# Kernel optimization log

Hardware: AMD Instinct MI355X
Metric: run time of the kernel (lower is better)

Reference implementation:

```python
import jax, jax.numpy as jnp
import numpy as np

BLOCK = 16
FP4_LEVELS = jnp.array([0.0, 0.5, 1.0, 1.5, 2.0, 3.0, 4.0, 6.0], dtype=jnp.float32)
FP4_MIDS = jnp.array([0.25, 0.75, 1.25, 1.75, 2.5, 3.5, 5.0], dtype=jnp.float32)
E4M3_MAX = 448.0
FP4_MAX = 6.0


def _fp4_round(v):
    # round-to-nearest onto signed E2M1 grid {0,.5,1,1.5,2,3,4,6}
    a = jnp.minimum(jnp.abs(v), FP4_MAX)
    idx = jnp.searchsorted(FP4_MIDS, a, side='right')
    return jnp.sign(v) * FP4_LEVELS[idx]


def _encode_scale(block_amax, global_amax):
    # two-level NVFP4 scaling: block scale stored as FP8 E4M3 relative to global scale
    g_scale = global_amax / (E4M3_MAX * FP4_MAX)
    s = block_amax / FP4_MAX
    s_q = jnp.clip(s / g_scale, 0.0, E4M3_MAX).astype(jnp.float8_e4m3fn).astype(jnp.float32) * g_scale
    return s_q


def nvfp4_qdq_1d(x, block=BLOCK):
    # blockwise fake-quant along the last dim (activations)
    sh = x.shape
    xb = x.reshape(sh[:-1] + (sh[-1] // block, block))
    g_amax = jnp.max(jnp.abs(x))
    b_amax = jnp.max(jnp.abs(xb), axis=-1, keepdims=True)
    s = _encode_scale(b_amax, g_amax)
    s_safe = jnp.where(s > 0, s, 1.0)
    dq = _fp4_round(xb / s_safe) * s
    return dq.reshape(sh)


def nvfp4_qdq_2d(w, block=BLOCK):
    # (16,16) 2D block fake-quant for the weight [out, in]
    O, I = w.shape
    wb = w.reshape(O // block, block, I // block, block)
    g_amax = jnp.max(jnp.abs(w))
    b_amax = jnp.max(jnp.abs(wb), axis=(1, 3), keepdims=True)
    s = _encode_scale(b_amax, g_amax)
    s_safe = jnp.where(s > 0, s, 1.0)
    dq = _fp4_round(wb / s_safe) * s
    return dq.reshape(O, I)


def setup_inputs() -> dict:
    key = jax.random.key(0)
    kx, kw = jax.random.split(key)
    B, S, D_IN, D_OUT = 4, 2048, 4096, 4096
    x = jax.random.normal(kx, (B, S, D_IN), dtype=jnp.float32)
    weight = jax.random.normal(kw, (D_OUT, D_IN), dtype=jnp.float32) * 0.02
    bias = jnp.zeros((D_OUT,), dtype=jnp.float32)
    return {"x": x, "weight": weight, "bias": bias}


def reference(x, weight, bias):
    x_hat = nvfp4_qdq_1d(x)
    x_ste = x + jax.lax.stop_gradient(x_hat - x)
    w_hat = nvfp4_qdq_2d(weight)
    w_ste = weight + jax.lax.stop_gradient(w_hat - weight)
    y = jnp.einsum('bsi,oi->bso', x_ste, w_ste)
    return y + bias
```

## Files before the change

### kernel.cpp

```cpp
#include <hip/hip_runtime.h>

typedef unsigned short u16;
typedef unsigned int u32;
typedef __bf16 bf16x8 __attribute__((ext_vector_type(8)));
typedef float f32x4 __attribute__((ext_vector_type(4)));


__device__ __forceinline__ float e4m3_rne(float r) {
  if (r < 0.015625f) {
    return rintf(r * 512.0f) * (1.0f / 512.0f);
  }
  u32 u = __float_as_uint(r);
  u32 lsb = (u >> 20) & 1u;
  u += 0x7FFFFu + lsb;
  u &= 0xFFF00000u;
  return __uint_as_float(u);
}

__device__ __forceinline__ float fp4_level(float a, const float* t) {
  return a < t[3] ? (a < t[1] ? (a < t[0] ? 0.0f : 0.5f)
                              : (a < t[2] ? 1.0f : 1.5f))
                  : (a < t[5] ? (a < t[4] ? 2.0f : 3.0f)
                              : (a < t[6] ? 4.0f : 6.0f));
}

__device__ __forceinline__ void gload_lds16(const u16* g, void* l) {
  __builtin_amdgcn_global_load_lds(
      (const __attribute__((address_space(1))) void*)g,
      (__attribute__((address_space(3))) void*)l, 16, 0, 0);
}


__global__ void __launch_bounds__(256) amax_part_kernel(const float4* __restrict__ p,
                                                        int n4, float* __restrict__ part) {
  float m = 0.0f;
  int stride = gridDim.x * 256;
  for (int i = blockIdx.x * 256 + threadIdx.x; i < n4; i += stride) {
    float4 v = p[i];
    m = fmaxf(m, fmaxf(fmaxf(fabsf(v.x), fabsf(v.y)), fmaxf(fabsf(v.z), fabsf(v.w))));
  }
#pragma unroll
  for (int o = 32; o > 0; o >>= 1) m = fmaxf(m, __shfl_xor(m, o));
  __shared__ float red[4];
  int wid = threadIdx.x >> 6, lane = threadIdx.x & 63;
  if (lane == 0) red[wid] = m;
  __syncthreads();
  if (threadIdx.x == 0)
    part[blockIdx.x] = fmaxf(fmaxf(red[0], red[1]), fmaxf(red[2], red[3]));
}

__global__ void __launch_bounds__(256) finalize_kernel(const float* __restrict__ px,
                                                       const float* __restrict__ pw,
                                                       float* __restrict__ scal,
                                                       int nx, int nw) {
  int tid = threadIdx.x;
  float mx = 0.0f, mw = 0.0f;
  for (int i = tid; i < nx; i += 256) mx = fmaxf(mx, px[i]);
  for (int i = tid; i < nw; i += 256) mw = fmaxf(mw, pw[i]);
#pragma unroll
  for (int o = 32; o > 0; o >>= 1) {
    mx = fmaxf(mx, __shfl_xor(mx, o));
    mw = fmaxf(mw, __shfl_xor(mw, o));
  }
  __shared__ float rx[4], rw[4];
  int wid = tid >> 6, lane = tid & 63;
  if (lane == 0) { rx[wid] = mx; rw[wid] = mw; }
  __syncthreads();
  if (tid == 0) {
    scal[0] = fmaxf(fmaxf(rx[0], rx[1]), fmaxf(rx[2], rx[3]));
    scal[1] = fmaxf(fmaxf(rw[0], rw[1]), fmaxf(rw[2], rw[3]));
  }
}


__global__ void __launch_bounds__(256) quant_x_kernel(const float* __restrict__ x,
                                                      const float* __restrict__ scal,
                                                      u16* __restrict__ q, int nblk) {
  int b = blockIdx.x * 256 + threadIdx.x;
  if (b >= nblk) return;
  const float4* px = (const float4*)(x + (size_t)b * 16);
  float4 v[4];
  v[0] = px[0]; v[1] = px[1]; v[2] = px[2]; v[3] = px[3];
  float am = 0.0f;
  const float* vf = (const float*)v;
#pragma unroll
  for (int i = 0; i < 16; ++i) am = fmaxf(am, fabsf(vf[i]));

  float g = scal[0] / 2688.0f;
  float ratio = fminf(fmaxf((am / 6.0f) / g, 0.0f), 448.0f);
  float sq = e4m3_rne(ratio);
  float s = sq * g;
  float ss = s > 0.0f ? s : 1.0f;
  float t[7] = {0.25f * ss, 0.75f * ss, 1.25f * ss, 1.75f * ss,
                2.5f * ss, 3.5f * ss, 5.0f * ss};

  union { u16 h[16]; uint4 v4[2]; } ou;
#pragma unroll
  for (int i = 0; i < 16; ++i) {
    float qv = copysignf(fp4_level(fabsf(vf[i]), t) * sq, vf[i]);
    ou.h[i] = (u16)(__float_as_uint(qv) >> 16);
  }
  uint4* qd = (uint4*)(q + (size_t)b * 16);
  qd[0] = ou.v4[0];
  qd[1] = ou.v4[1];
}


__global__ void __launch_bounds__(256) quant_w_kernel(const float* __restrict__ w,
                                                      const float* __restrict__ scal,
                                                      u16* __restrict__ q, int ntc, int K) {
  int wav = blockIdx.x * 4 + (threadIdx.x >> 6);
  int lane = threadIdx.x & 63;
  int tr = wav / ntc, tc = wav % ntc;
  int r = lane >> 2, c = (lane & 3) * 4;
  size_t off = (size_t)(tr * 16 + r) * K + tc * 16 + c;
  float4 v = *(const float4*)(w + off);
  float am = fmaxf(fmaxf(fabsf(v.x), fabsf(v.y)), fmaxf(fabsf(v.z), fabsf(v.w)));
#pragma unroll
  for (int o = 32; o > 0; o >>= 1) am = fmaxf(am, __shfl_xor(am, o));

  float g = scal[1] / 2688.0f;
  float ratio = fminf(fmaxf((am / 6.0f) / g, 0.0f), 448.0f);
  float sq = e4m3_rne(ratio);
  float s = sq * g;
  float ss = s > 0.0f ? s : 1.0f;
  float t[7] = {0.25f * ss, 0.75f * ss, 1.25f * ss, 1.75f * ss,
                2.5f * ss, 3.5f * ss, 5.0f * ss};

  float vf[4] = {v.x, v.y, v.z, v.w};
  union { u16 h[4]; uint2 v2; } ou;
#pragma unroll
  for (int i = 0; i < 4; ++i) {
    float qv = copysignf(fp4_level(fabsf(vf[i]), t) * sq, vf[i]);
    ou.h[i] = (u16)(__float_as_uint(qv) >> 16);
  }
  *(uint2*)(q + off) = ou.v2;
}


#define BM 256
#define BN 256
#define BK 64

__global__ void __launch_bounds__(512, 2) gemm_kernel(const u16* __restrict__ A,
                                                      const u16* __restrict__ B,
                                                      const float* __restrict__ bias,
                                                      const float* __restrict__ scal,
                                                      float* __restrict__ out,
                                                      int M, int N, int K) {
  extern __shared__ char lds[];
  const int tid = threadIdx.x;
  const int wid = tid >> 6, lane = tid & 63;
  const int fr = lane & 15, fc = lane >> 4;
  const int wm = wid >> 2, wn = wid & 3;
  const int sw = (fr & 7) << 4;

  int nwg = gridDim.x, bid = blockIdx.x;
  int q8 = nwg >> 3, r8 = nwg & 7;
  int xcd = bid & 7, loc = bid >> 3;
  int wg = (xcd < r8 ? xcd * (q8 + 1) : r8 * (q8 + 1) + (xcd - r8) * q8) + loc;
  int ntn = N / BN;
  int tm = wg / ntn, tn = wg % ntn;
  int brow = tm * BM, bcol = tn * BN;

  const int srow = tid >> 3;
  const int scol = ((((tid & 7) << 4) ^ ((srow & 7) << 4)) >> 1);
  const u16* gA = A + (size_t)(brow + srow) * K + scol;
  const u16* gB = B + (size_t)(bcol + srow) * K + scol;
  const size_t K64 = (size_t)K * 64;
  const int ldsOff = wid << 10;

#define STAGE_A(bufbase, ktoff) do {                                         \
    _Pragma("unroll") for (int s_ = 0; s_ < 4; ++s_)                         \
      gload_lds16(gA + (size_t)s_ * K64 + (ktoff), (bufbase) + s_ * 8192 + ldsOff); \
  } while (0)
#define STAGE_B(bufbase, ktoff) do {                                         \
    _Pragma("unroll") for (int s_ = 0; s_ < 4; ++s_)                         \
      gload_lds16(gB + (size_t)s_ * K64 + (ktoff), (bufbase) + s_ * 8192 + ldsOff); \
  } while (0)

#define LOAD_A(dst, qm)                                                      \
  _Pragma("unroll") for (int j_ = 0; j_ < 4; ++j_)                           \
  _Pragma("unroll") for (int k_ = 0; k_ < 2; ++k_)                           \
    dst[j_][k_] = *(const bf16x8*)(abuf + ((wm * 128 + (qm) * 64 + j_ * 16 + fr) * 128 \
                                           + (((fc << 4) + (k_ << 6)) ^ sw)));
#define LOAD_B(dst, qn)                                                      \
  _Pragma("unroll") for (int j_ = 0; j_ < 2; ++j_)                           \
  _Pragma("unroll") for (int k_ = 0; k_ < 2; ++k_)                           \
    dst[j_][k_] = *(const bf16x8*)(bbuf + ((wn * 64 + (qn) * 32 + j_ * 16 + fr) * 128 \
                                           + (((fc << 4) + (k_ << 6)) ^ sw)));

#define MMA(qm, qn, af, bf)                                                  \
  _Pragma("unroll") for (int j_ = 0; j_ < 4; ++j_)                           \
  _Pragma("unroll") for (int n_ = 0; n_ < 2; ++n_)                           \
  _Pragma("unroll") for (int k_ = 0; k_ < 2; ++k_)                           \
    acc[(qm) * 4 + j_][(qn) * 2 + n_] = __builtin_amdgcn_mfma_f32_16x16x32_bf16( \
        af[j_][k_], bf[n_][k_], acc[(qm) * 4 + j_][(qn) * 2 + n_], 0, 0, 0);

#define PHASE_MID()                                          \
  __builtin_amdgcn_s_barrier();                              \
  asm volatile("s_waitcnt lgkmcnt(0)" ::: "memory");         \
  __builtin_amdgcn_sched_barrier(0);                         \
  __builtin_amdgcn_s_setprio(1);
#define PHASE_END()                                          \
  __builtin_amdgcn_s_setprio(0);                             \
  __builtin_amdgcn_s_barrier();

  f32x4 acc[8][4];
  f32x4 zero = {0.0f, 0.0f, 0.0f, 0.0f};
#pragma unroll
  for (int m = 0; m < 8; ++m)
#pragma unroll
    for (int n = 0; n < 4; ++n) acc[m][n] = zero;

  const int NT = K / BK;

  STAGE_A(lds, 0);
  STAGE_B(lds + 32768, 0);
  asm volatile("s_waitcnt vmcnt(0)" ::: "memory");
  __builtin_amdgcn_s_barrier();

  bf16x8 a[4][2], b0[2][2], b1[2][2];
  int cur = 0;
  for (int t = 0; t < NT; ++t) {
    const char* abuf = lds + cur * 65536;
    const char* bbuf = abuf + 32768;
    char* sbuf = lds + (cur ^ 1) * 65536;
    const bool pf = (t + 1 < NT);
    const int ktn = (t + 1) * BK;

    LOAD_A(a, 0);
    LOAD_B(b0, 0);
    if (pf) STAGE_A(sbuf, ktn);
    PHASE_MID();
    MMA(0, 0, a, b0);
    PHASE_END();

    LOAD_B(b1, 1);
    if (pf) STAGE_B(sbuf + 32768, ktn);
    PHASE_MID();
    MMA(0, 1, a, b1);
    PHASE_END();

    LOAD_A(a, 1);
    PHASE_MID();
    MMA(1, 1, a, b1);
    PHASE_END();

    __builtin_amdgcn_s_setprio(1);
    MMA(1, 0, a, b0);
    __builtin_amdgcn_s_setprio(0);
    asm volatile("s_waitcnt vmcnt(0)" ::: "memory");
    __builtin_amdgcn_s_barrier();
    cur ^= 1;
  }

  float gs = (scal[0] / 2688.0f) * (scal[1] / 2688.0f);
#pragma unroll
  for (int n = 0; n < 4; ++n) {
    int col = bcol + wn * 64 + n * 16 + fr;
    float bv = bias[col];
#pragma unroll
    for (int m = 0; m < 8; ++m) {
      int row0 = brow + wm * 128 + m * 16 + (fc << 2);
      f32x4 v = acc[m][n];
#pragma unroll
      for (int j = 0; j < 4; ++j)
        out[(size_t)(row0 + j) * N + col] = v[j] * gs + bv;
    }
  }
}


extern "C" void kernel_launch(void* const* d_in, const int* in_sizes, int n_in,
                              void* d_out, int out_size, void* d_ws, size_t ws_size,
                              hipStream_t stream) {
  const float* x = (const float*)d_in[0];
  const float* w = (const float*)d_in[1];
  const float* bias = (const float*)d_in[2];
  float* out = (float*)d_out;

  const int DOUT = in_sizes[2];
  const int K = in_sizes[1] / DOUT;
  const int M = in_sizes[0] / K;
  const int N = DOUT;

  float* scal = (float*)d_ws;
  float* px = (float*)((char*)d_ws + 256);
  float* pw = px + 1024;
  u16* qw = (u16*)((char*)d_ws + 8192);
  u16* qx = (u16*)((char*)d_ws + 8192 + (size_t)N * K * 2);

  amax_part_kernel<<<1024, 256, 0, stream>>>((const float4*)x, (M * K) / 4, px);
  amax_part_kernel<<<512, 256, 0, stream>>>((const float4*)w, (N * K) / 4, pw);
  finalize_kernel<<<1, 256, 0, stream>>>(px, pw, scal, 1024, 512);

  int nblk = (M * K) / 16;
  quant_x_kernel<<<(nblk + 255) / 256, 256, 0, stream>>>(x, scal, qx, nblk);

  int ntiles = (N / 16) * (K / 16);
  quant_w_kernel<<<ntiles / 4, 256, 0, stream>>>(w, scal, qw, K / 16, K);

  gemm_kernel<<<(M / BM) * (N / BN), 512, 131072, stream>>>(qx, qw, bias, scal, out,
                                                            M, N, K);
}
```

Before: 348.6 us.

## Replace direct global-to-LDS loads with register-staged prefetch in GEMM mainloop

Drops the global_load_lds direct-to-LDS staging in the bf16 MFMA GEMM. Tiles are now loaded into registers (uint4), then written to the swizzled LDS buffer in the third phase, and the final loop iteration is peeled. The end-of-iteration vmcnt wait and barrier are removed, and B fragments are reloaded before the last MMA so the register budget stays manageable. The aim is to hide global latency behind MFMA work without a full vmcnt stall per tile, at the cost of extra VGPRs and LDS write instructions.

New measurement: 458.0 us. 1.31x slower.

```diff
diff --git a/kernel.cpp b/kernel.cpp
--- a/kernel.cpp
+++ b/kernel.cpp
@@ -22,12 +22,6 @@
                               : (a < t[2] ? 1.0f : 1.5f))
                   : (a < t[5] ? (a < t[4] ? 2.0f : 3.0f)
                               : (a < t[6] ? 4.0f : 6.0f));
-}
-
-__device__ __forceinline__ void gload_lds16(const u16* g, void* l) {
-  __builtin_amdgcn_global_load_lds(
-      (const __attribute__((address_space(1))) void*)g,
-      (__attribute__((address_space(3))) void*)l, 16, 0, 0);
 }
 
 
@@ -164,19 +158,25 @@
   int brow = tm * BM, bcol = tn * BN;
 
   const int srow = tid >> 3;
-  const int scol = ((((tid & 7) << 4) ^ ((srow & 7) << 4)) >> 1);
-  const u16* gA = A + (size_t)(brow + srow) * K + scol;
-  const u16* gB = B + (size_t)(bcol + srow) * K + scol;
+  const u16* gA = A + (size_t)(brow + srow) * K + (tid & 7) * 8;
+  const u16* gB = B + (size_t)(bcol + srow) * K + (tid & 7) * 8;
   const size_t K64 = (size_t)K * 64;
-  const int ldsOff = wid << 10;
-
-#define STAGE_A(bufbase, ktoff) do {                                         \
-    _Pragma("unroll") for (int s_ = 0; s_ < 4; ++s_)                         \
-      gload_lds16(gA + (size_t)s_ * K64 + (ktoff), (bufbase) + s_ * 8192 + ldsOff); \
+  const int wOff = srow * 128 + (((tid & 7) << 4) ^ ((srow & 7) << 4));
+
+  uint4 ra[4], rb[4];
+#define GLOAD_A(kt) do {                                                     \
+    _Pragma("unroll") for (int c_ = 0; c_ < 4; ++c_)                         \
+      ra[c_] = *(const uint4*)(gA + (size_t)c_ * K64 + (kt));                \
   } while (0)
-#define STAGE_B(bufbase, ktoff) do {                                         \
-    _Pragma("unroll") for (int s_ = 0; s_ < 4; ++s_)                         \
-      gload_lds16(gB + (size_t)s_ * K64 + (ktoff), (bufbase) + s_ * 8192 + ldsOff); \
+#define GLOAD_B(kt) do {                                                     \
+    _Pragma("unroll") for (int c_ = 0; c_ < 4; ++c_)                         \
+      rb[c_] = *(const uint4*)(gB + (size_t)c_ * K64 + (kt));                \
+  } while (0)
+#define SWRITE(bufbase) do {                                                 \
+    _Pragma("unroll") for (int c_ = 0; c_ < 4; ++c_)                         \
+      *(uint4*)((bufbase) + c_ * 8192 + wOff) = ra[c_];                      \
+    _Pragma("unroll") for (int c_ = 0; c_ < 4; ++c_)                         \
+      *(uint4*)((bufbase) + 32768 + c_ * 8192 + wOff) = rb[c_];              \
   } while (0)
 
 #define LOAD_A(dst, qm)                                                      \
@@ -204,7 +204,8 @@
   __builtin_amdgcn_s_setprio(1);
 #define PHASE_END()                                          \
   __builtin_amdgcn_s_setprio(0);                             \
-  __builtin_amdgcn_s_barrier();
+  __builtin_amdgcn_s_barrier();                              \
+  __builtin_amdgcn_sched_barrier(0);
 
   f32x4 acc[8][4];
   f32x4 zero = {0.0f, 0.0f, 0.0f, 0.0f};
@@ -215,44 +216,69 @@
 
   const int NT = K / BK;
 
-  STAGE_A(lds, 0);
-  STAGE_B(lds + 32768, 0);
-  asm volatile("s_waitcnt vmcnt(0)" ::: "memory");
-  __builtin_amdgcn_s_barrier();
+  GLOAD_A(0);
+  GLOAD_B(0);
+  SWRITE(lds);
+  __syncthreads();
 
   bf16x8 a[4][2], b0[2][2], b1[2][2];
   int cur = 0;
-  for (int t = 0; t < NT; ++t) {
+  for (int t = 0; t < NT - 1; ++t) {
     const char* abuf = lds + cur * 65536;
     const char* bbuf = abuf + 32768;
     char* sbuf = lds + (cur ^ 1) * 65536;
-    const bool pf = (t + 1 < NT);
     const int ktn = (t + 1) * BK;
 
     LOAD_A(a, 0);
     LOAD_B(b0, 0);
-    if (pf) STAGE_A(sbuf, ktn);
+    GLOAD_A(ktn);
     PHASE_MID();
     MMA(0, 0, a, b0);
     PHASE_END();
 
     LOAD_B(b1, 1);
-    if (pf) STAGE_B(sbuf + 32768, ktn);
+    GLOAD_B(ktn);
     PHASE_MID();
     MMA(0, 1, a, b1);
     PHASE_END();
 
     LOAD_A(a, 1);
+    SWRITE(sbuf);
     PHASE_MID();
     MMA(1, 1, a, b1);
     PHASE_END();
 
+    LOAD_B(b0, 0);
+    asm volatile("s_waitcnt lgkmcnt(0)" ::: "memory");
+    __builtin_amdgcn_sched_barrier(0);
     __builtin_amdgcn_s_setprio(1);
     MMA(1, 0, a, b0);
     __builtin_amdgcn_s_setprio(0);
-    asm volatile("s_waitcnt vmcnt(0)" ::: "memory");
-    __builtin_amdgcn_s_barrier();
     cur ^= 1;
+  }
+
+  {
+    const char* abuf = lds + cur * 65536;
+    const char* bbuf = abuf + 32768;
+    LOAD_A(a, 0);
+    LOAD_B(b0, 0);
+    PHASE_MID();
+    MMA(0, 0, a, b0);
+    PHASE_END();
+    LOAD_B(b1, 1);
+    PHASE_MID();
+    MMA(0, 1, a, b1);
+    PHASE_END();
+    LOAD_A(a, 1);
+    PHASE_MID();
+    MMA(1, 1, a, b1);
+    PHASE_END();
+    LOAD_B(b0, 0);
+    asm volatile("s_waitcnt lgkmcnt(0)" ::: "memory");
+    __builtin_amdgcn_sched_barrier(0);
+    __builtin_amdgcn_s_setprio(1);
+    MMA(1, 0, a, b0);
+    __builtin_amdgcn_s_setprio(0);
   }
 
   float gs = (scal[0] / 2688.0f) * (scal[1] / 2688.0f);
```

## Stage global-to-LDS loads in finer chunks two tiles ahead with partial vmcnt waits

Applied to the files above, without the earlier changes.

Splits the A and B global-to-LDS staging into per-chunk loads. Part of the next-next tile's data is issued into the buffer currently being consumed, once its rows are no longer needed. Waits become partial vmcnt waits instead of full drains, and LDS reads use inline ds_read_b128 with immediate offsets to cut address arithmetic. B staging also gets a new row layout matching the per-wave quadrant reads. This deepens the prefetch to hide global latency, at the cost of delicate correctness reasoning around buffer reuse and wait counts.

After: 335.2 us. 1.04x faster.

```diff
diff --git a/kernel.cpp b/kernel.cpp
--- a/kernel.cpp
+++ b/kernel.cpp
@@ -166,29 +166,45 @@
   const int srow = tid >> 3;
   const int scol = ((((tid & 7) << 4) ^ ((srow & 7) << 4)) >> 1);
   const u16* gA = A + (size_t)(brow + srow) * K + scol;
-  const u16* gB = B + (size_t)(bcol + srow) * K + scol;
-  const size_t K64 = (size_t)K * 64;
-  const int ldsOff = wid << 10;
-
-#define STAGE_A(bufbase, ktoff) do {                                         \
-    _Pragma("unroll") for (int s_ = 0; s_ < 4; ++s_)                         \
-      gload_lds16(gA + (size_t)s_ * K64 + (ktoff), (bufbase) + s_ * 8192 + ldsOff); \
-  } while (0)
-#define STAGE_B(bufbase, ktoff) do {                                         \
-    _Pragma("unroll") for (int s_ = 0; s_ < 4; ++s_)                         \
-      gload_lds16(gB + (size_t)s_ * K64 + (ktoff), (bufbase) + s_ * 8192 + ldsOff); \
-  } while (0)
-
-#define LOAD_A(dst, qm)                                                      \
-  _Pragma("unroll") for (int j_ = 0; j_ < 4; ++j_)                           \
-  _Pragma("unroll") for (int k_ = 0; k_ < 2; ++k_)                           \
-    dst[j_][k_] = *(const bf16x8*)(abuf + ((wm * 128 + (qm) * 64 + j_ * 16 + fr) * 128 \
-                                           + (((fc << 4) + (k_ << 6)) ^ sw)));
-#define LOAD_B(dst, qn)                                                      \
-  _Pragma("unroll") for (int j_ = 0; j_ < 2; ++j_)                           \
-  _Pragma("unroll") for (int k_ = 0; k_ < 2; ++k_)                           \
-    dst[j_][k_] = *(const bf16x8*)(bbuf + ((wn * 64 + (qn) * 32 + j_ * 16 + fr) * 128 \
-                                           + (((fc << 4) + (k_ << 6)) ^ sw)));
+  const int rowB0 = (srow & 31) + (srow >> 5) * 128;
+  const u16* gB = B + (size_t)(bcol + rowB0) * K + scol;
+  const size_t K64r = (size_t)K * 64;
+  const size_t K32r = (size_t)K * 32;
+  const int ldsAoff = wid << 10;
+  const int ldsBoff = ((wid & 3) << 10) + ((wid >> 2) << 14);
+
+#define STAGE_A1(buf, kt, c) \
+  gload_lds16(gA + (size_t)(c) * K64r + (kt), (buf) + (c) * 8192 + ldsAoff)
+#define STAGE_B1(buf, kt, c) \
+  gload_lds16(gB + (size_t)(c) * K32r + (kt), (buf) + 32768 + (c) * 4096 + ldsBoff)
+
+  const u32 ldsbase = (u32)(uintptr_t)(__attribute__((address_space(3))) char*)lds;
+  const u32 cb0 = (u32)((fc << 4) ^ sw);
+  const u32 cb1 = cb0 ^ 64u;
+  const u32 aB0 = ldsbase + (u32)((wm * 128 + fr) * 128) + cb0;
+  const u32 aB1 = ldsbase + (u32)((wm * 128 + fr) * 128) + cb1;
+  const u32 bB0 = ldsbase + 32768u + (u32)((wn * 64 + fr) * 128) + cb0;
+  const u32 bB1 = ldsbase + 32768u + (u32)((wn * 64 + fr) * 128) + cb1;
+
+#define DSR(dst, ad, off) \
+  asm volatile("ds_read_b128 %0, %1 offset:" off : "=v"(dst) : "v"(ad))
+
+#define LOAD_A0() do { \
+  DSR(a[0][0], aC0, "0");    DSR(a[0][1], aC1, "0");    \
+  DSR(a[1][0], aC0, "2048"); DSR(a[1][1], aC1, "2048"); \
+  DSR(a[2][0], aC0, "4096"); DSR(a[2][1], aC1, "4096"); \
+  DSR(a[3][0], aC0, "6144"); DSR(a[3][1], aC1, "6144"); } while (0)
+#define LOAD_A1() do { \
+  DSR(a[0][0], aC0, "8192");  DSR(a[0][1], aC1, "8192");  \
+  DSR(a[1][0], aC0, "10240"); DSR(a[1][1], aC1, "10240"); \
+  DSR(a[2][0], aC0, "12288"); DSR(a[2][1], aC1, "12288"); \
+  DSR(a[3][0], aC0, "14336"); DSR(a[3][1], aC1, "14336"); } while (0)
+#define LOAD_B0() do { \
+  DSR(b0[0][0], bC0, "0");    DSR(b0[0][1], bC1, "0");    \
+  DSR(b0[1][0], bC0, "2048"); DSR(b0[1][1], bC1, "2048"); } while (0)
+#define LOAD_B1() do { \
+  DSR(b1[0][0], bC0, "4096"); DSR(b1[0][1], bC1, "4096"); \
+  DSR(b1[1][0], bC0, "6144"); DSR(b1[1][1], bC1, "6144"); } while (0)
 
 #define MMA(qm, qn, af, bf)                                                  \
   _Pragma("unroll") for (int j_ = 0; j_ < 4; ++j_)                           \
@@ -204,7 +220,8 @@
   __builtin_amdgcn_s_setprio(1);
 #define PHASE_END()                                          \
   __builtin_amdgcn_s_setprio(0);                             \
-  __builtin_amdgcn_s_barrier();
+  __builtin_amdgcn_s_barrier();                              \
+  __builtin_amdgcn_sched_barrier(0);
 
   f32x4 acc[8][4];
   f32x4 zero = {0.0f, 0.0f, 0.0f, 0.0f};
@@ -215,43 +232,54 @@
 
   const int NT = K / BK;
 
-  STAGE_A(lds, 0);
-  STAGE_B(lds + 32768, 0);
-  asm volatile("s_waitcnt vmcnt(0)" ::: "memory");
+  STAGE_A1(lds, 0, 0); STAGE_A1(lds, 0, 1); STAGE_A1(lds, 0, 2); STAGE_A1(lds, 0, 3);
+  STAGE_B1(lds, 0, 0); STAGE_B1(lds, 0, 1); STAGE_B1(lds, 0, 2); STAGE_B1(lds, 0, 3);
+  STAGE_A1(lds + 65536, BK, 0); STAGE_A1(lds + 65536, BK, 2);
+  STAGE_B1(lds + 65536, BK, 1); STAGE_B1(lds + 65536, BK, 3);
+  asm volatile("s_waitcnt vmcnt(4)" ::: "memory");
   __builtin_amdgcn_s_barrier();
 
   bf16x8 a[4][2], b0[2][2], b1[2][2];
   int cur = 0;
   for (int t = 0; t < NT; ++t) {
-    const char* abuf = lds + cur * 65536;
-    const char* bbuf = abuf + 32768;
-    char* sbuf = lds + (cur ^ 1) * 65536;
-    const bool pf = (t + 1 < NT);
-    const int ktn = (t + 1) * BK;
-
-    LOAD_A(a, 0);
-    LOAD_B(b0, 0);
-    if (pf) STAGE_A(sbuf, ktn);
+    const u32 bo = (u32)(cur << 16);
+    const u32 aC0 = aB0 + bo, aC1 = aB1 + bo;
+    const u32 bC0 = bB0 + bo, bC1 = bB1 + bo;
+    char* bq = lds + (cur ^ 1) * 65536;
+    char* bp = lds + cur * 65536;
+    const int kt1 = (t + 1) * BK, kt2 = (t + 2) * BK;
+    const int st1 = (t + 1 < NT), st2 = (t + 2 < NT);
+
+    LOAD_A0();
+    LOAD_B0();
+    if (st1) { STAGE_A1(bq, kt1, 1); STAGE_A1(bq, kt1, 3); }
     PHASE_MID();
     MMA(0, 0, a, b0);
     PHASE_END();
 
-    LOAD_B(b1, 1);
-    if (pf) STAGE_B(sbuf + 32768, ktn);
+    LOAD_B1();
+    if (st1) { STAGE_B1(bq, kt1, 0); STAGE_B1(bq, kt1, 2); }
     PHASE_MID();
     MMA(0, 1, a, b1);
-    PHASE_END();
-
-    LOAD_A(a, 1);
+    __builtin_amdgcn_s_setprio(0);
+    asm volatile("s_waitcnt vmcnt(4)" ::: "memory");
+    __builtin_amdgcn_s_barrier();
+    __builtin_amdgcn_sched_barrier(0);
+
+    LOAD_A1();
+    if (st2) { STAGE_A1(bp, kt2, 0); STAGE_A1(bp, kt2, 2); }
     PHASE_MID();
     MMA(1, 1, a, b1);
     PHASE_END();
 
+    if (st2) { STAGE_B1(bp, kt2, 1); STAGE_B1(bp, kt2, 3); }
     __builtin_amdgcn_s_setprio(1);
     MMA(1, 0, a, b0);
     __builtin_amdgcn_s_setprio(0);
-    asm volatile("s_waitcnt vmcnt(0)" ::: "memory");
+    if (st2) asm volatile("s_waitcnt vmcnt(4)" ::: "memory");
+    else     asm volatile("s_waitcnt vmcnt(0)" ::: "memory");
     __builtin_amdgcn_s_barrier();
+    __builtin_amdgcn_sched_barrier(0);
     cur ^= 1;
   }
 
```

## Restructure GEMM mainloop into 4-stage BK=32 pipeline with register double-buffering

Applied to the files above, without the earlier changes.

Halves the K tile to 32 and uses four LDS stages, prefetching two tiles ahead with partial vmcnt waits instead of draining all loads every iteration. LDS reads for the next tile are issued with inline ds_read_b128 into a second register set, between the two MMA halves, so fragment loads overlap with MFMA work. It also switches to a new swizzled LDS layout with two rows per 128-byte line. The aim is to remove per-iteration barrier stalls and global-load latency exposure, at the cost of more register pressure and more barriers per unit of K.

After: 359.4 us. 3.1% more time.

```diff
diff --git a/kernel.cpp b/kernel.cpp
--- a/kernel.cpp
+++ b/kernel.cpp
@@ -140,7 +140,7 @@
 
 #define BM 256
 #define BN 256
-#define BK 64
+#define BK 32
 
 __global__ void __launch_bounds__(512, 2) gemm_kernel(const u16* __restrict__ A,
                                                       const u16* __restrict__ B,
@@ -153,7 +153,6 @@
   const int wid = tid >> 6, lane = tid & 63;
   const int fr = lane & 15, fc = lane >> 4;
   const int wm = wid >> 2, wn = wid & 3;
-  const int sw = (fr & 7) << 4;
 
   int nwg = gridDim.x, bid = blockIdx.x;
   int q8 = nwg >> 3, r8 = nwg & 7;
@@ -163,48 +162,72 @@
   int tm = wg / ntn, tn = wg % ntn;
   int brow = tm * BM, bcol = tn * BN;
 
-  const int srow = tid >> 3;
-  const int scol = ((((tid & 7) << 4) ^ ((srow & 7) << 4)) >> 1);
-  const u16* gA = A + (size_t)(brow + srow) * K + scol;
-  const u16* gB = B + (size_t)(bcol + srow) * K + scol;
-  const size_t K64 = (size_t)K * 64;
-  const int ldsOff = wid << 10;
-
-#define STAGE_A(bufbase, ktoff) do {                                         \
-    _Pragma("unroll") for (int s_ = 0; s_ < 4; ++s_)                         \
-      gload_lds16(gA + (size_t)s_ * K64 + (ktoff), (bufbase) + s_ * 8192 + ldsOff); \
+  {
+  }
+  const int j0 = tid >> 3, s0 = tid & 7;
+  const int x0 = s0 ^ (j0 & 7);
+  const int grow0 = 2 * j0 + (x0 >> 2);
+  const int gk0 = (x0 & 3) * 8;
+  const u16* gA0 = A + (size_t)(brow + grow0) * K + gk0;
+  const u16* gB0 = B + (size_t)(bcol + grow0) * K + gk0;
+  const size_t K128 = (size_t)K * 128;
+
+#define STAGE(tt) do {                                                        \
+    const int kt_ = (tt) * BK;                                                \
+    char* bb_ = lds + (((tt) & 3) << 15);                                     \
+    gload_lds16(gA0 + kt_, bb_ + tid * 16);                                   \
+    gload_lds16(gA0 + K128 + kt_, bb_ + 8192 + tid * 16);                     \
+    gload_lds16(gB0 + kt_, bb_ + 16384 + tid * 16);                           \
+    gload_lds16(gB0 + K128 + kt_, bb_ + 24576 + tid * 16);                    \
   } while (0)
-#define STAGE_B(bufbase, ktoff) do {                                         \
-    _Pragma("unroll") for (int s_ = 0; s_ < 4; ++s_)                         \
-      gload_lds16(gB + (size_t)s_ * K64 + (ktoff), (bufbase) + s_ * 8192 + ldsOff); \
+
+  const u32 ldsbase = (u32)(uintptr_t)(__attribute__((address_space(3))) char*)lds;
+  const u32 slot = (u32)(((((fr & 1) << 2) | fc) ^ ((fr >> 1) & 7)) << 4);
+  const u32 aBase = ldsbase + (u32)((wm * 64 + (fr >> 1)) * 128) + slot;
+  const u32 bBase = ldsbase + 16384u + (u32)((wn * 32 + (fr >> 1)) * 128) + slot;
+
+#define DSR(dst, ad, off) \
+  asm volatile("ds_read_b128 %0, %1 offset:" off : "=v"(dst) : "v"(ad))
+
+#define READ(tt, da, db) do {                                                 \
+    const u32 bo_ = (u32)(((tt) & 3) << 15);                                  \
+    const u32 aA_ = aBase + bo_, bA_ = bBase + bo_;                           \
+    DSR(da[0], aA_, "0");    DSR(da[1], aA_, "1024");                         \
+    DSR(da[2], aA_, "2048"); DSR(da[3], aA_, "3072");                         \
+    DSR(da[4], aA_, "4096"); DSR(da[5], aA_, "5120");                         \
+    DSR(da[6], aA_, "6144"); DSR(da[7], aA_, "7168");                         \
+    DSR(db[0], bA_, "0");    DSR(db[1], bA_, "1024");                         \
+    DSR(db[2], bA_, "2048"); DSR(db[3], bA_, "3072");                         \
   } while (0)
 
-#define LOAD_A(dst, qm)                                                      \
-  _Pragma("unroll") for (int j_ = 0; j_ < 4; ++j_)                           \
-  _Pragma("unroll") for (int k_ = 0; k_ < 2; ++k_)                           \
-    dst[j_][k_] = *(const bf16x8*)(abuf + ((wm * 128 + (qm) * 64 + j_ * 16 + fr) * 128 \
-                                           + (((fc << 4) + (k_ << 6)) ^ sw)));
-#define LOAD_B(dst, qn)                                                      \
-  _Pragma("unroll") for (int j_ = 0; j_ < 2; ++j_)                           \
-  _Pragma("unroll") for (int k_ = 0; k_ < 2; ++k_)                           \
-    dst[j_][k_] = *(const bf16x8*)(bbuf + ((wn * 64 + (qn) * 32 + j_ * 16 + fr) * 128 \
-                                           + (((fc << 4) + (k_ << 6)) ^ sw)));
-
-#define MMA(qm, qn, af, bf)                                                  \
-  _Pragma("unroll") for (int j_ = 0; j_ < 4; ++j_)                           \
-  _Pragma("unroll") for (int n_ = 0; n_ < 2; ++n_)                           \
-  _Pragma("unroll") for (int k_ = 0; k_ < 2; ++k_)                           \
-    acc[(qm) * 4 + j_][(qn) * 2 + n_] = __builtin_amdgcn_mfma_f32_16x16x32_bf16( \
-        af[j_][k_], bf[n_][k_], acc[(qm) * 4 + j_][(qn) * 2 + n_], 0, 0, 0);
-
-#define PHASE_MID()                                          \
-  __builtin_amdgcn_s_barrier();                              \
+#define MMA_HALF(ca, cb, mh)                                                  \
+  _Pragma("unroll") for (int m_ = 0; m_ < 4; ++m_)                            \
+  _Pragma("unroll") for (int n_ = 0; n_ < 4; ++n_)                            \
+    acc[(mh) + m_][n_] = __builtin_amdgcn_mfma_f32_16x16x32_bf16(             \
+        ca[(mh) + m_], cb[n_], acc[(mh) + m_][n_], 0, 0, 0);
+
+#define WAITK0()                                             \
   asm volatile("s_waitcnt lgkmcnt(0)" ::: "memory");         \
-  __builtin_amdgcn_sched_barrier(0);                         \
-  __builtin_amdgcn_s_setprio(1);
-#define PHASE_END()                                          \
-  __builtin_amdgcn_s_setprio(0);                             \
-  __builtin_amdgcn_s_barrier();
+  __builtin_amdgcn_sched_barrier(0);
+#define VMC(n)                                               \
+  asm volatile("s_waitcnt vmcnt(" #n ")" ::: "memory");      \
+  __builtin_amdgcn_sched_barrier(0);
+
+#define BODY(tt, ca, cb, na, nb) do {                                         \
+    if ((tt) + 2 < NT) STAGE((tt) + 2);                                       \
+    WAITK0();                                                                 \
+    __builtin_amdgcn_s_setprio(1);                                            \
+    MMA_HALF(ca, cb, 0);                                                      \
+    __builtin_amdgcn_s_setprio(0);                                            \
+    if ((tt) + 2 < NT) { VMC(4); } else { VMC(0); }                           \
+    __builtin_amdgcn_s_barrier();                                             \
+    __builtin_amdgcn_sched_barrier(0);                                        \
+    if ((tt) + 1 < NT) READ((tt) + 1, na, nb);                                \
+    __builtin_amdgcn_s_setprio(1);                                            \
+    MMA_HALF(ca, cb, 4);                                                      \
+    __builtin_amdgcn_s_setprio(0);                                            \
+    __builtin_amdgcn_sched_barrier(0);                                        \
+  } while (0)
 
   f32x4 acc[8][4];
   f32x4 zero = {0.0f, 0.0f, 0.0f, 0.0f};
@@ -215,44 +238,16 @@
 
   const int NT = K / BK;
 
-  STAGE_A(lds, 0);
-  STAGE_B(lds + 32768, 0);
-  asm volatile("s_waitcnt vmcnt(0)" ::: "memory");
+  STAGE(0);
+  STAGE(1);
+  VMC(4);
   __builtin_amdgcn_s_barrier();
-
-  bf16x8 a[4][2], b0[2][2], b1[2][2];
-  int cur = 0;
-  for (int t = 0; t < NT; ++t) {
-    const char* abuf = lds + cur * 65536;
-    const char* bbuf = abuf + 32768;
-    char* sbuf = lds + (cur ^ 1) * 65536;
-    const bool pf = (t + 1 < NT);
-    const int ktn = (t + 1) * BK;
-
-    LOAD_A(a, 0);
-    LOAD_B(b0, 0);
-    if (pf) STAGE_A(sbuf, ktn);
-    PHASE_MID();
-    MMA(0, 0, a, b0);
-    PHASE_END();
-
-    LOAD_B(b1, 1);
-    if (pf) STAGE_B(sbuf + 32768, ktn);
-    PHASE_MID();
-    MMA(0, 1, a, b1);
-    PHASE_END();
-
-    LOAD_A(a, 1);
-    PHASE_MID();
-    MMA(1, 1, a, b1);
-    PHASE_END();
-
-    __builtin_amdgcn_s_setprio(1);
-    MMA(1, 0, a, b0);
-    __builtin_amdgcn_s_setprio(0);
-    asm volatile("s_waitcnt vmcnt(0)" ::: "memory");
-    __builtin_amdgcn_s_barrier();
-    cur ^= 1;
+  bf16x8 aP[8], bP[4], aQ[8], bQ[4];
+  READ(0, aP, bP);
+
+  for (int t = 0; t < NT; t += 2) {
+    BODY(t, aP, bP, aQ, bQ);
+    BODY(t + 1, aQ, bQ, aP, bP);
   }
 
   float gs = (scal[0] / 2688.0f) * (scal[1] / 2688.0f);
```
